# Optimization experiments

Measured on AMD Instinct MI355X. Metric: run time of the kernel, lower is better.

Reference implementation:

```python
import jax, jax.numpy as jnp
import numpy as np

D_MODEL, N_HEADS, D_K, D_V = 512, 8, 32, 32
LN_EPS = 1e-5


def setup_inputs() -> dict:
    key = jax.random.key(0)
    ks = jax.random.split(key, 12)
    B, L = 4, 2048
    inner = N_HEADS * D_K
    s_in = 1.0 / np.sqrt(D_MODEL)
    s_fc = 1.0 / np.sqrt(inner)
    return {
        "q": jax.random.normal(ks[0], (B, L, D_MODEL), jnp.float32),
        "k": jax.random.normal(ks[1], (B, L, D_MODEL), jnp.float32),
        "v": jax.random.normal(ks[2], (B, L, D_MODEL), jnp.float32),
        "Wq": jax.random.normal(ks[3], (inner, D_MODEL), jnp.float32) * s_in,
        "bq": jax.random.normal(ks[4], (inner,), jnp.float32) * 0.01,
        "Wk": jax.random.normal(ks[5], (inner, D_MODEL), jnp.float32) * s_in,
        "bk": jax.random.normal(ks[6], (inner,), jnp.float32) * 0.01,
        "Wv": jax.random.normal(ks[7], (N_HEADS * D_V, D_MODEL), jnp.float32) * s_in,
        "bv": jax.random.normal(ks[8], (N_HEADS * D_V,), jnp.float32) * 0.01,
        "Wfc": jax.random.normal(ks[9], (D_MODEL, N_HEADS * D_V), jnp.float32) * s_fc,
        "bfc": jax.random.normal(ks[10], (D_MODEL,), jnp.float32) * 0.01,
        "gamma": jnp.ones((D_MODEL,), jnp.float32),
        "beta": jnp.zeros((D_MODEL,), jnp.float32),
    }


def reference(q, k, v, Wq, bq, Wk, bk, Wv, bv, Wfc, bfc, gamma, beta):
    n, l, _ = q.shape
    # Projection output interpreted as (..., d_k, n_heads): head idx is fastest dim
    def split_heads(x, W, b, dh):
        p = x @ W.T + b                     # [n, l, dh*H]
        return p.reshape(n, x.shape[1], dh, N_HEADS).transpose(0, 3, 1, 2)  # [n,H,l,dh]

    qh = split_heads(q, Wq, bq, D_K)
    kh = split_heads(k, Wk, bk, D_K)
    vh = split_heads(v, Wv, bv, D_V)

    scale = 1.0 / jnp.sqrt(jnp.asarray(D_K, q.dtype))
    scores = jnp.einsum('nhqd,nhkd->nhqk', qh, kh) * scale  # [n,H,L,L]
    att = jax.nn.softmax(scores, axis=-1)
    out = jnp.einsum('nhqk,nhkd->nhqd', att, vh)             # [n,H,L,d_v]
    out = out.transpose(0, 2, 1, 3).reshape(n, l, N_HEADS * D_V)

    fc = out @ Wfc.T + bfc
    x = fc + q  # residual
    mean = jnp.mean(x, axis=-1, keepdims=True)
    var = jnp.mean(jnp.square(x - mean), axis=-1, keepdims=True)
    return gamma * (x - mean) / jnp.sqrt(var + LN_EPS) + beta
```

## Files before the change

kernel.cpp:

```cpp
#include <hip/hip_runtime.h>
#include <math.h>

constexpr int Bn = 4, Ln = 2048, DM = 512, NH = 8, DKv = 32, INNER = 256;
constexpr int TTOK = Bn * Ln;
constexpr size_t HEAD_ELEMS = (size_t)Bn * NH * Ln * DKv;


typedef short short8 __attribute__((ext_vector_type(8)));
typedef short short4v __attribute__((ext_vector_type(4)));
typedef float floatx4 __attribute__((ext_vector_type(4)));
typedef float floatx16 __attribute__((ext_vector_type(16)));

constexpr size_t WB_OFF  = 12536832;
constexpr size_t WFCB_OFF = WB_OFF + 3 * 131072;

constexpr float C1 = 0.25505654f;

__device__ inline short f2bf(float x) {
  unsigned u = __builtin_bit_cast(unsigned, x);
  unsigned r = (u + 0x7FFFu + ((u >> 16) & 1u)) >> 16;
  return (short)r;
}

__global__ __launch_bounds__(256) void cvtw_kernel(
    const float* __restrict__ Wq, const float* __restrict__ Wk,
    const float* __restrict__ Wv, const float* __restrict__ Wfc,
    short* __restrict__ Wb, short* __restrict__ Wfcb)
{
  const int z = blockIdx.y;
  const float* src = z == 0 ? Wq : (z == 1 ? Wk : (z == 2 ? Wv : Wfc));
  short* dst = z < 3 ? Wb + (size_t)z * 131072 : Wfcb;
  const int idx = (blockIdx.x * 256 + threadIdx.x) * 4;
  float4 x = *(const float4*)&src[idx];
  *(short4v*)&dst[idx] = (short4v){f2bf(x.x), f2bf(x.y), f2bf(x.z), f2bf(x.w)};
}

__global__ __launch_bounds__(256) void proj_kernel(
    const float* __restrict__ q, const float* __restrict__ k, const float* __restrict__ v,
    const short* __restrict__ Wb,
    const float* __restrict__ bq, const float* __restrict__ bk,
    const float* __restrict__ bv,
    short* __restrict__ ws)
{
  const int mat = blockIdx.y;
  const float* X    = mat == 0 ? q  : (mat == 1 ? k  : v);
  const short* W    = Wb + (size_t)mat * 131072;
  const float* bias = mat == 0 ? bq : (mat == 1 ? bk : bv);
  short* outp = ws + (size_t)mat * HEAD_ELEMS;

  const int t0 = blockIdx.x * 64;
  const int tid = threadIdx.x;
  const int col = tid & 15;
  const int quad = (tid & 63) >> 4;
  const int w = tid >> 6;

  __shared__ short smem[23040];
  short* Xs  = smem;
  short* Wsh = smem + 64 * 72;

  floatx16 accv;
  floatx4 acc[16];
#pragma unroll
  for (int nj = 0; nj < 16; ++nj) acc[nj] = (floatx4){0.f, 0.f, 0.f, 0.f};
  (void)accv;

  float4 xr[4];
  short8 wr[8];
  auto loadX = [&](int k0) {
#pragma unroll
    for (int j = 0; j < 4; ++j) {
      const int i = tid + j * 256, row = i >> 4, c4 = i & 15;
      xr[j] = *(const float4*)&X[(size_t)(t0 + row) * DM + k0 + c4 * 4];
    }
  };
  auto loadW = [&](int k0) {
#pragma unroll
    for (int j = 0; j < 8; ++j) {
      const int s = tid + j * 256, jrow = s >> 3, c8 = s & 7;
      const int wrow = ((jrow & 31) << 3) + (jrow >> 5);
      wr[j] = *(const short8*)&W[(size_t)wrow * DM + k0 + c8 * 8];
    }
  };

  loadX(0);
  loadW(0);

  for (int kc = 0; kc < 8; ++kc) {
#pragma unroll
    for (int j = 0; j < 4; ++j) {
      const int i = tid + j * 256, row = i >> 4, c4 = i & 15;
      *(short4v*)&Xs[row * 72 + c4 * 4] =
          (short4v){f2bf(xr[j].x), f2bf(xr[j].y), f2bf(xr[j].z), f2bf(xr[j].w)};
    }
#pragma unroll
    for (int j = 0; j < 8; ++j) {
      const int s = tid + j * 256, jrow = s >> 3, c8 = s & 7;
      *(short8*)&Wsh[jrow * 72 + c8 * 8] = wr[j];
    }
    __syncthreads();
    if (kc < 7) {
      loadX((kc + 1) * 64);
      loadW((kc + 1) * 64);
    }
#pragma unroll
    for (int ks = 0; ks < 2; ++ks) {
      short8 a = *(const short8*)&Xs[(w * 16 + col) * 72 + ks * 32 + quad * 8];
#pragma unroll
      for (int nj = 0; nj < 16; ++nj) {
        short8 b = *(const short8*)&Wsh[(nj * 16 + col) * 72 + ks * 32 + quad * 8];
        acc[nj] = __builtin_amdgcn_mfma_f32_16x16x32_bf16(a, b, acc[nj], 0, 0, 0);
      }
    }
    __syncthreads();
  }

  short* Ct = smem;
  const int n = t0 >> 11, llb = t0 & (Ln - 1);

  if (mat < 2) {
#pragma unroll
    for (int nj = 0; nj < 16; ++nj) {
      const int j = nj * 16 + col;
      const int c = ((j & 31) << 3) + (j >> 5);
      const float bi = bias[c];
#pragma unroll
      for (int r = 0; r < 4; ++r) {
        float pv = acc[nj][r] + bi;
        if (mat == 0) pv *= C1;
        Ct[(w * 16 + quad * 4 + r) * 268 + j] = f2bf(pv);
      }
    }
    __syncthreads();
#pragma unroll
    for (int it = 0; it < 8; ++it) {
      const int cid = tid + it * 256;
      const int h = cid >> 8, tok = (cid >> 2) & 63, o = cid & 3;
      short8 val = *(const short8*)&Ct[tok * 268 + h * 32 + o * 8];
      *(short8*)&outp[((size_t)(n * NH + h) * Ln + llb + tok) * DKv + o * 8] = val;
    }
  } else {
#pragma unroll
    for (int nj = 0; nj < 16; ++nj) {
      const int j = nj * 16 + col;
      const int c = ((j & 31) << 3) + (j >> 5);
      const float bi = bias[c];
      short4v pk = (short4v){f2bf(acc[nj][0] + bi), f2bf(acc[nj][1] + bi),
                             f2bf(acc[nj][2] + bi), f2bf(acc[nj][3] + bi)};
      *(short4v*)&Ct[j * 72 + w * 16 + quad * 4] = pk;
    }
    __syncthreads();
#pragma unroll
    for (int it = 0; it < 8; ++it) {
      const int cid = tid + it * 256;
      const int j = cid >> 3, to = cid & 7;
      const int h = j >> 5, d = j & 31;
      short8 val = *(const short8*)&Ct[j * 72 + to * 8];
      *(short8*)&outp[((size_t)(n * NH + h) * DKv + d) * Ln + llb + to * 8] = val;
    }
  }
}

__global__ __launch_bounds__(256) void attn_kernel(const short* __restrict__ ws,
                                                   short* __restrict__ O2b)
{
  const int vid = blockIdx.x + 16 * blockIdx.y;
  const int xcd = vid & 7, jj = vid >> 3;
  const int bh = xcd * 4 + (jj >> 4);
  const int qblk = jj & 15;

  const int n = bh >> 3, h = bh & 7;
  const int tid = threadIdx.x;
  const int lane = tid & 63;
  const int col = lane & 31;
  const int hf = lane >> 5;
  const int w = tid >> 6;
  const int qi = qblk * 128 + w * 32 + col;

  const short* Qh = ws;
  const short* Kg = ws + HEAD_ELEMS + (size_t)bh * Ln * DKv;
  const short* Vg = ws + 2 * HEAD_ELEMS + (size_t)bh * DKv * Ln;

  __shared__ short Ks[2][128 * 40];
  __shared__ short Vs[2][32 * 136];

  short8 aq[2];
#pragma unroll
  for (int c = 0; c < 2; ++c)
    aq[c] = *(const short8*)&Qh[(size_t)bh * Ln * DKv + (size_t)qi * DKv + c * 16 + hf * 8];

  short8 ones;
#pragma unroll
  for (int j = 0; j < 8; ++j) ones[j] = (short)0x3F80;

  floatx16 o, ol;
#pragma unroll
  for (int i = 0; i < 16; ++i) { o[i] = 0.f; ol[i] = 0.f; }

  const int kg = tid >> 1, khalf = tid & 1;
  const int krow = (kg & ~12) | ((kg & 4) << 1) | ((kg & 8) >> 1);
  const int kst = krow * 40 + khalf * 16;
  const int vd = tid >> 3, vkb = tid & 7;
  const int vst = vd * 136 + vkb * 16;

  short8 kr0 = *(const short8*)(Kg + kg * 32 + khalf * 16);
  short8 kr1 = *(const short8*)(Kg + kg * 32 + khalf * 16 + 8);
  short8 vr0 = *(const short8*)(Vg + (size_t)vd * Ln + vkb * 16);
  short8 vr1 = *(const short8*)(Vg + (size_t)vd * Ln + vkb * 16 + 8);

  for (int kt = 0; kt < 16; ++kt) {
    short* ksb = Ks[kt & 1];
    short* vsb = Vs[kt & 1];
    *(short8*)&ksb[kst] = kr0;
    *(short8*)&ksb[kst + 8] = kr1;
    *(short8*)&vsb[vst] = vr0;
    *(short8*)&vsb[vst + 8] = vr1;
    __syncthreads();
    if (kt < 15) {
      kr0 = *(const short8*)(Kg + (size_t)(kt + 1) * 4096 + kg * 32 + khalf * 16);
      kr1 = *(const short8*)(Kg + (size_t)(kt + 1) * 4096 + kg * 32 + khalf * 16 + 8);
      vr0 = *(const short8*)(Vg + (size_t)vd * Ln + (kt + 1) * 128 + vkb * 16);
      vr1 = *(const short8*)(Vg + (size_t)vd * Ln + (kt + 1) * 128 + vkb * 16 + 8);
    }

#pragma unroll
    for (int cc = 0; cc < 4; ++cc) {
      floatx16 st;
#pragma unroll
      for (int i = 0; i < 16; ++i) st[i] = 0.f;
      short8 kf0 = *(const short8*)&ksb[(cc * 32 + col) * 40 + hf * 8];
      short8 kf1 = *(const short8*)&ksb[(cc * 32 + col) * 40 + 16 + hf * 8];
      st = __builtin_amdgcn_mfma_f32_32x32x16_bf16(kf0, aq[0], st, 0, 0, 0);
      st = __builtin_amdgcn_mfma_f32_32x32x16_bf16(kf1, aq[1], st, 0, 0, 0);

      float p[16];
#pragma unroll
      for (int i = 0; i < 16; ++i) p[i] = __builtin_amdgcn_exp2f(st[i]);
      short8 pf[2];
#pragma unroll
      for (int half = 0; half < 2; ++half) {
        unsigned u[4];
#pragma unroll
        for (int j = 0; j < 4; ++j)
          u[j] = __builtin_amdgcn_perm(
              __builtin_bit_cast(unsigned, p[half * 8 + 2 * j + 1]),
              __builtin_bit_cast(unsigned, p[half * 8 + 2 * j]), 0x07060302u);
        uint4 uu = make_uint4(u[0], u[1], u[2], u[3]);
        pf[half] = __builtin_bit_cast(short8, uu);
      }

      ol = __builtin_amdgcn_mfma_f32_32x32x16_bf16(ones, pf[0], ol, 0, 0, 0);
      ol = __builtin_amdgcn_mfma_f32_32x32x16_bf16(ones, pf[1], ol, 0, 0, 0);

      short8 va0 = *(const short8*)&vsb[col * 136 + cc * 32 + hf * 8];
      short8 va1 = *(const short8*)&vsb[col * 136 + cc * 32 + 16 + hf * 8];
      o = __builtin_amdgcn_mfma_f32_32x32x16_bf16(va0, pf[0], o, 0, 0, 0);
      o = __builtin_amdgcn_mfma_f32_32x32x16_bf16(va1, pf[1], o, 0, 0, 0);
    }
  }

  const float inv = 1.f / ol[0];
  short* dst = &O2b[((size_t)n * Ln + qi) * INNER + h * DKv];
#pragma unroll
  for (int g4 = 0; g4 < 4; ++g4) {
    short4v pk = (short4v){f2bf(o[g4 * 4 + 0] * inv), f2bf(o[g4 * 4 + 1] * inv),
                           f2bf(o[g4 * 4 + 2] * inv), f2bf(o[g4 * 4 + 3] * inv)};
    *(short4v*)&dst[8 * g4 + 4 * hf] = pk;
  }
}

__global__ __launch_bounds__(256) void fcln_kernel(
    const short* __restrict__ O2b, const short* __restrict__ Wfcb,
    const float* __restrict__ bfc, const float* __restrict__ qin,
    const float* __restrict__ gamma, const float* __restrict__ beta,
    float* __restrict__ outp)
{
  const int t0 = blockIdx.x * 16;
  const int tid = threadIdx.x;
  const int col = tid & 15;
  const int quad = (tid & 63) >> 4;
  const int w = tid >> 6;

  __shared__ short As[16 * 264];
  __shared__ float sred[2][16][4];

  {
    const int row = tid >> 4, k16 = tid & 15;
    *(short8*)&As[row * 264 + k16 * 16] =
        *(const short8*)&O2b[(size_t)(t0 + row) * INNER + k16 * 16];
    *(short8*)&As[row * 264 + k16 * 16 + 8] =
        *(const short8*)&O2b[(size_t)(t0 + row) * INNER + k16 * 16 + 8];
  }
  __syncthreads();

  const short* Wp = Wfcb + (size_t)(w * 128 + col) * INNER + quad * 8;

  floatx4 acc[8];
#pragma unroll
  for (int nj = 0; nj < 8; ++nj) acc[nj] = (floatx4){0.f, 0.f, 0.f, 0.f};

#pragma unroll
  for (int ks = 0; ks < 8; ++ks) {
    short8 a = *(const short8*)&As[col * 264 + ks * 32 + quad * 8];
#pragma unroll
    for (int nj = 0; nj < 8; ++nj) {
      short8 b = *(const short8*)&Wp[(size_t)nj * 16 * INNER + ks * 32];
      acc[nj] = __builtin_amdgcn_mfma_f32_16x16x32_bf16(a, b, acc[nj], 0, 0, 0);
    }
  }

  float s1[4], s2[4];
#pragma unroll
  for (int r = 0; r < 4; ++r) { s1[r] = 0.f; s2[r] = 0.f; }

#pragma unroll
  for (int nj = 0; nj < 8; ++nj) {
    const int c = w * 128 + nj * 16 + col;
    const float bi = bfc[c];
#pragma unroll
    for (int r = 0; r < 4; ++r) {
      const int t = t0 + quad * 4 + r;
      float x = acc[nj][r] + bi + qin[(size_t)t * DM + c];
      acc[nj][r] = x;
      s1[r] += x;
      s2[r] += x * x;
    }
  }
#pragma unroll
  for (int r = 0; r < 4; ++r) {
#pragma unroll
    for (int off = 1; off <= 8; off <<= 1) {
      s1[r] += __shfl_xor(s1[r], off);
      s2[r] += __shfl_xor(s2[r], off);
    }
  }
  if (col == 0) {
#pragma unroll
    for (int r = 0; r < 4; ++r) {
      sred[0][quad * 4 + r][w] = s1[r];
      sred[1][quad * 4 + r][w] = s2[r];
    }
  }
  __syncthreads();

  float mean[4], rstd[4];
#pragma unroll
  for (int r = 0; r < 4; ++r) {
    const int tk = quad * 4 + r;
    const float S1 = sred[0][tk][0] + sred[0][tk][1] + sred[0][tk][2] + sred[0][tk][3];
    const float S2 = sred[1][tk][0] + sred[1][tk][1] + sred[1][tk][2] + sred[1][tk][3];
    mean[r] = S1 * (1.f / 512.f);
    const float var = S2 * (1.f / 512.f) - mean[r] * mean[r];
    rstd[r] = rsqrtf(var + 1e-5f);
  }

#pragma unroll
  for (int nj = 0; nj < 8; ++nj) {
    const int c = w * 128 + nj * 16 + col;
    const float g = gamma[c], bb = beta[c];
#pragma unroll
    for (int r = 0; r < 4; ++r) {
      const int t = t0 + quad * 4 + r;
      outp[(size_t)t * DM + c] = g * (acc[nj][r] - mean[r]) * rstd[r] + bb;
    }
  }
}

extern "C" void kernel_launch(void* const* d_in, const int* in_sizes, int n_in,
                              void* d_out, int out_size, void* d_ws, size_t ws_size,
                              hipStream_t stream) {
  const float* q     = (const float*)d_in[0];
  const float* k     = (const float*)d_in[1];
  const float* v     = (const float*)d_in[2];
  const float* Wq    = (const float*)d_in[3];
  const float* bq    = (const float*)d_in[4];
  const float* Wk    = (const float*)d_in[5];
  const float* bk    = (const float*)d_in[6];
  const float* Wv    = (const float*)d_in[7];
  const float* bv    = (const float*)d_in[8];
  const float* Wfc   = (const float*)d_in[9];
  const float* bfc   = (const float*)d_in[10];
  const float* gamma = (const float*)d_in[11];
  const float* beta  = (const float*)d_in[12];

  short* wsS  = (short*)d_ws;
  short* O2b  = wsS + 3 * HEAD_ELEMS;
  short* Wb   = wsS + WB_OFF;
  short* Wfcb = wsS + WFCB_OFF;

  cvtw_kernel<<<dim3(128, 4), 256, 0, stream>>>(Wq, Wk, Wv, Wfc, Wb, Wfcb);

  dim3 gp(TTOK / 64, 3);
  proj_kernel<<<gp, 256, 0, stream>>>(q, k, v, Wb, bq, bk, bv, wsS);

  dim3 gatt(Ln / 128, Bn * NH);
  attn_kernel<<<gatt, 256, 0, stream>>>(wsS, O2b);

  fcln_kernel<<<dim3(TTOK / 16), 256, 0, stream>>>(O2b, Wfcb, bfc, q, gamma, beta,
                                                   (float*)d_out);
}
```

Baseline: 174.5 us.

## Fuse four kernels into one cooperative persistent kernel with grid syncs

Replaces the weight-convert, projection, attention and FC+LayerNorm launches with a single cooperative kernel of 512 blocks that runs the four stages in sequence, separated by grid-wide barriers. Block indices are remapped per stage, and the attention stage spreads heads across XCDs. The aim is to remove launch gaps and tail effects between kernels. In exchange, every stage is limited to 512 blocks, and the grid syncs add barrier cost. If the cooperative launch fails, the code falls back to the old four-kernel path.

```diff
diff --git a/kernel.cpp b/kernel.cpp
--- a/kernel.cpp
+++ b/kernel.cpp
@@ -1,5 +1,8 @@
 #include <hip/hip_runtime.h>
+#include <hip/hip_cooperative_groups.h>
 #include <math.h>
+
+namespace cg = cooperative_groups;
 
 constexpr int Bn = 4, Ln = 2048, DM = 512, NH = 8, DKv = 32, INNER = 256;
 constexpr int TTOK = Bn * Ln;
@@ -20,6 +23,354 @@
   unsigned u = __builtin_bit_cast(unsigned, x);
   unsigned r = (u + 0x7FFFu + ((u >> 16) & 1u)) >> 16;
   return (short)r;
+}
+
+__global__ __launch_bounds__(256, 2) void mega_kernel(
+    const float* __restrict__ q, const float* __restrict__ kin,
+    const float* __restrict__ vin,
+    const float* __restrict__ Wq, const float* __restrict__ Wk,
+    const float* __restrict__ Wv, const float* __restrict__ Wfc,
+    const float* __restrict__ bq, const float* __restrict__ bk,
+    const float* __restrict__ bv, const float* __restrict__ bfc,
+    const float* __restrict__ gamma, const float* __restrict__ beta,
+    short* __restrict__ wsS, float* __restrict__ outp)
+{
+  cg::grid_group grid = cg::this_grid();
+  const int u = blockIdx.x;
+  const int tid = threadIdx.x;
+
+  short* Wb   = wsS + WB_OFF;
+  short* Wfcb = wsS + WFCB_OFF;
+  short* O2b  = wsS + 3 * HEAD_ELEMS;
+
+  __shared__ __align__(16) short smem[23040];
+
+  {
+    const int z = u >> 7, xb = u & 127;
+    const float* src = z == 0 ? Wq : (z == 1 ? Wk : (z == 2 ? Wv : Wfc));
+    short* dst = z < 3 ? Wb + (size_t)z * 131072 : Wfcb;
+    const int idx = (xb * 256 + tid) * 4;
+    float4 x = *(const float4*)&src[idx];
+    *(short4v*)&dst[idx] = (short4v){f2bf(x.x), f2bf(x.y), f2bf(x.z), f2bf(x.w)};
+  }
+  grid.sync();
+
+  if (u < 384) {
+    const int mat = u >> 7;
+    const int t0 = (u & 127) * 64;
+    const float* X    = mat == 0 ? q  : (mat == 1 ? kin : vin);
+    const short* W    = Wb + (size_t)mat * 131072;
+    const float* bias = mat == 0 ? bq : (mat == 1 ? bk : bv);
+    short* outph = wsS + (size_t)mat * HEAD_ELEMS;
+
+    const int col = tid & 15;
+    const int quad = (tid & 63) >> 4;
+    const int w = tid >> 6;
+
+    short* Xs  = smem;
+    short* Wsh = smem + 64 * 72;
+
+    floatx4 acc[16];
+#pragma unroll
+    for (int nj = 0; nj < 16; ++nj) acc[nj] = (floatx4){0.f, 0.f, 0.f, 0.f};
+
+    float4 xr[4];
+    short8 wr[8];
+    auto loadX = [&](int k0) {
+#pragma unroll
+      for (int j = 0; j < 4; ++j) {
+        const int i = tid + j * 256, row = i >> 4, c4 = i & 15;
+        xr[j] = *(const float4*)&X[(size_t)(t0 + row) * DM + k0 + c4 * 4];
+      }
+    };
+    auto loadW = [&](int k0) {
+#pragma unroll
+      for (int j = 0; j < 8; ++j) {
+        const int s = tid + j * 256, jrow = s >> 3, c8 = s & 7;
+        const int wrow = ((jrow & 31) << 3) + (jrow >> 5);
+        wr[j] = *(const short8*)&W[(size_t)wrow * DM + k0 + c8 * 8];
+      }
+    };
+
+    loadX(0);
+    loadW(0);
+
+    for (int kc = 0; kc < 8; ++kc) {
+#pragma unroll
+      for (int j = 0; j < 4; ++j) {
+        const int i = tid + j * 256, row = i >> 4, c4 = i & 15;
+        *(short4v*)&Xs[row * 72 + c4 * 4] =
+            (short4v){f2bf(xr[j].x), f2bf(xr[j].y), f2bf(xr[j].z), f2bf(xr[j].w)};
+      }
+#pragma unroll
+      for (int j = 0; j < 8; ++j) {
+        const int s = tid + j * 256, jrow = s >> 3, c8 = s & 7;
+        *(short8*)&Wsh[jrow * 72 + c8 * 8] = wr[j];
+      }
+      __syncthreads();
+      if (kc < 7) {
+        loadX((kc + 1) * 64);
+        loadW((kc + 1) * 64);
+      }
+#pragma unroll
+      for (int ks = 0; ks < 2; ++ks) {
+        short8 a = *(const short8*)&Xs[(w * 16 + col) * 72 + ks * 32 + quad * 8];
+#pragma unroll
+        for (int nj = 0; nj < 16; ++nj) {
+          short8 b = *(const short8*)&Wsh[(nj * 16 + col) * 72 + ks * 32 + quad * 8];
+          acc[nj] = __builtin_amdgcn_mfma_f32_16x16x32_bf16(a, b, acc[nj], 0, 0, 0);
+        }
+      }
+      __syncthreads();
+    }
+
+    short* Ct = smem;
+    const int n = t0 >> 11, llb = t0 & (Ln - 1);
+
+    if (mat < 2) {
+#pragma unroll
+      for (int nj = 0; nj < 16; ++nj) {
+        const int j = nj * 16 + col;
+        const int c = ((j & 31) << 3) + (j >> 5);
+        const float bi = bias[c];
+#pragma unroll
+        for (int r = 0; r < 4; ++r) {
+          float pv = acc[nj][r] + bi;
+          if (mat == 0) pv *= C1;
+          Ct[(w * 16 + quad * 4 + r) * 268 + j] = f2bf(pv);
+        }
+      }
+      __syncthreads();
+#pragma unroll
+      for (int it = 0; it < 8; ++it) {
+        const int cid = tid + it * 256;
+        const int h = cid >> 8, tok = (cid >> 2) & 63, o = cid & 3;
+        short8 val = *(const short8*)&Ct[tok * 268 + h * 32 + o * 8];
+        *(short8*)&outph[((size_t)(n * NH + h) * Ln + llb + tok) * DKv + o * 8] = val;
+      }
+    } else {
+#pragma unroll
+      for (int nj = 0; nj < 16; ++nj) {
+        const int j = nj * 16 + col;
+        const int c = ((j & 31) << 3) + (j >> 5);
+        const float bi = bias[c];
+        short4v pk = (short4v){f2bf(acc[nj][0] + bi), f2bf(acc[nj][1] + bi),
+                               f2bf(acc[nj][2] + bi), f2bf(acc[nj][3] + bi)};
+        *(short4v*)&Ct[j * 72 + w * 16 + quad * 4] = pk;
+      }
+      __syncthreads();
+#pragma unroll
+      for (int it = 0; it < 8; ++it) {
+        const int cid = tid + it * 256;
+        const int j = cid >> 3, to = cid & 7;
+        const int h = j >> 5, d = j & 31;
+        short8 val = *(const short8*)&Ct[j * 72 + to * 8];
+        *(short8*)&outph[((size_t)(n * NH + h) * DKv + d) * Ln + llb + to * 8] = val;
+      }
+    }
+  }
+  grid.sync();
+
+  {
+    const int vid = u;
+    const int xcd = vid & 7, jj = vid >> 3;
+    const int bh = xcd * 4 + (jj >> 4);
+    const int qblk = jj & 15;
+
+    const int n = bh >> 3, h = bh & 7;
+    const int lane = tid & 63;
+    const int col = lane & 31;
+    const int hf = lane >> 5;
+    const int w = tid >> 6;
+    const int qi = qblk * 128 + w * 32 + col;
+
+    const short* Qh = wsS;
+    const short* Kg = wsS + HEAD_ELEMS + (size_t)bh * Ln * DKv;
+    const short* Vg = wsS + 2 * HEAD_ELEMS + (size_t)bh * DKv * Ln;
+
+    short8 aq[2];
+#pragma unroll
+    for (int c = 0; c < 2; ++c)
+      aq[c] = *(const short8*)&Qh[(size_t)bh * Ln * DKv + (size_t)qi * DKv + c * 16 + hf * 8];
+
+    short8 ones;
+#pragma unroll
+    for (int j = 0; j < 8; ++j) ones[j] = (short)0x3F80;
+
+    floatx16 o, ol;
+#pragma unroll
+    for (int i = 0; i < 16; ++i) { o[i] = 0.f; ol[i] = 0.f; }
+
+    const int kg = tid >> 1, khalf = tid & 1;
+    const int krow = (kg & ~12) | ((kg & 4) << 1) | ((kg & 8) >> 1);
+    const int kst = krow * 40 + khalf * 16;
+    const int vd = tid >> 3, vkb = tid & 7;
+    const int vst = vd * 136 + vkb * 16;
+
+    short8 kr0 = *(const short8*)(Kg + kg * 32 + khalf * 16);
+    short8 kr1 = *(const short8*)(Kg + kg * 32 + khalf * 16 + 8);
+    short8 vr0 = *(const short8*)(Vg + (size_t)vd * Ln + vkb * 16);
+    short8 vr1 = *(const short8*)(Vg + (size_t)vd * Ln + vkb * 16 + 8);
+
+    for (int kt = 0; kt < 16; ++kt) {
+      short* ksb = smem + (kt & 1) * 5120;
+      short* vsb = smem + 10240 + (kt & 1) * 4352;
+      *(short8*)&ksb[kst] = kr0;
+      *(short8*)&ksb[kst + 8] = kr1;
+      *(short8*)&vsb[vst] = vr0;
+      *(short8*)&vsb[vst + 8] = vr1;
+      __syncthreads();
+      if (kt < 15) {
+        kr0 = *(const short8*)(Kg + (size_t)(kt + 1) * 4096 + kg * 32 + khalf * 16);
+        kr1 = *(const short8*)(Kg + (size_t)(kt + 1) * 4096 + kg * 32 + khalf * 16 + 8);
+        vr0 = *(const short8*)(Vg + (size_t)vd * Ln + (kt + 1) * 128 + vkb * 16);
+        vr1 = *(const short8*)(Vg + (size_t)vd * Ln + (kt + 1) * 128 + vkb * 16 + 8);
+      }
+
+#pragma unroll
+      for (int cc = 0; cc < 4; ++cc) {
+        floatx16 st;
+#pragma unroll
+        for (int i = 0; i < 16; ++i) st[i] = 0.f;
+        short8 kf0 = *(const short8*)&ksb[(cc * 32 + col) * 40 + hf * 8];
+        short8 kf1 = *(const short8*)&ksb[(cc * 32 + col) * 40 + 16 + hf * 8];
+        st = __builtin_amdgcn_mfma_f32_32x32x16_bf16(kf0, aq[0], st, 0, 0, 0);
+        st = __builtin_amdgcn_mfma_f32_32x32x16_bf16(kf1, aq[1], st, 0, 0, 0);
+
+        float p[16];
+#pragma unroll
+        for (int i = 0; i < 16; ++i) p[i] = __builtin_amdgcn_exp2f(st[i]);
+        short8 pf[2];
+#pragma unroll
+        for (int half = 0; half < 2; ++half) {
+          unsigned uu0 = __builtin_amdgcn_perm(
+              __builtin_bit_cast(unsigned, p[half * 8 + 1]),
+              __builtin_bit_cast(unsigned, p[half * 8 + 0]), 0x07060302u);
+          unsigned uu1 = __builtin_amdgcn_perm(
+              __builtin_bit_cast(unsigned, p[half * 8 + 3]),
+              __builtin_bit_cast(unsigned, p[half * 8 + 2]), 0x07060302u);
+          unsigned uu2 = __builtin_amdgcn_perm(
+              __builtin_bit_cast(unsigned, p[half * 8 + 5]),
+              __builtin_bit_cast(unsigned, p[half * 8 + 4]), 0x07060302u);
+          unsigned uu3 = __builtin_amdgcn_perm(
+              __builtin_bit_cast(unsigned, p[half * 8 + 7]),
+              __builtin_bit_cast(unsigned, p[half * 8 + 6]), 0x07060302u);
+          uint4 uu = make_uint4(uu0, uu1, uu2, uu3);
+          pf[half] = __builtin_bit_cast(short8, uu);
+        }
+
+        ol = __builtin_amdgcn_mfma_f32_32x32x16_bf16(ones, pf[0], ol, 0, 0, 0);
+        ol = __builtin_amdgcn_mfma_f32_32x32x16_bf16(ones, pf[1], ol, 0, 0, 0);
+
+        short8 va0 = *(const short8*)&vsb[col * 136 + cc * 32 + hf * 8];
+        short8 va1 = *(const short8*)&vsb[col * 136 + cc * 32 + 16 + hf * 8];
+        o = __builtin_amdgcn_mfma_f32_32x32x16_bf16(va0, pf[0], o, 0, 0, 0);
+        o = __builtin_amdgcn_mfma_f32_32x32x16_bf16(va1, pf[1], o, 0, 0, 0);
+      }
+    }
+
+    const float inv = 1.f / ol[0];
+    short* dst = &O2b[((size_t)n * Ln + qi) * INNER + h * DKv];
+#pragma unroll
+    for (int g4 = 0; g4 < 4; ++g4) {
+      short4v pk = (short4v){f2bf(o[g4 * 4 + 0] * inv), f2bf(o[g4 * 4 + 1] * inv),
+                             f2bf(o[g4 * 4 + 2] * inv), f2bf(o[g4 * 4 + 3] * inv)};
+      *(short4v*)&dst[8 * g4 + 4 * hf] = pk;
+    }
+  }
+  grid.sync();
+
+  {
+    const int t0 = u * 16;
+    const int col = tid & 15;
+    const int quad = (tid & 63) >> 4;
+    const int w = tid >> 6;
+
+    short* As = smem;
+    float* sred = (float*)(smem + 4224);
+
+    {
+      const int row = tid >> 4, k16 = tid & 15;
+      *(short8*)&As[row * 264 + k16 * 16] =
+          *(const short8*)&O2b[(size_t)(t0 + row) * INNER + k16 * 16];
+      *(short8*)&As[row * 264 + k16 * 16 + 8] =
+          *(const short8*)&O2b[(size_t)(t0 + row) * INNER + k16 * 16 + 8];
+    }
+    __syncthreads();
+
+    const short* Wp = Wfcb + (size_t)(w * 128 + col) * INNER + quad * 8;
+
+    floatx4 acc[8];
+#pragma unroll
+    for (int nj = 0; nj < 8; ++nj) acc[nj] = (floatx4){0.f, 0.f, 0.f, 0.f};
+
+#pragma unroll
+    for (int ks = 0; ks < 8; ++ks) {
+      short8 a = *(const short8*)&As[col * 264 + ks * 32 + quad * 8];
+#pragma unroll
+      for (int nj = 0; nj < 8; ++nj) {
+        short8 b = *(const short8*)&Wp[(size_t)nj * 16 * INNER + ks * 32];
+        acc[nj] = __builtin_amdgcn_mfma_f32_16x16x32_bf16(a, b, acc[nj], 0, 0, 0);
+      }
+    }
+
+    float s1[4], s2[4];
+#pragma unroll
+    for (int r = 0; r < 4; ++r) { s1[r] = 0.f; s2[r] = 0.f; }
+
+#pragma unroll
+    for (int nj = 0; nj < 8; ++nj) {
+      const int c = w * 128 + nj * 16 + col;
+      const float bi = bfc[c];
+#pragma unroll
+      for (int r = 0; r < 4; ++r) {
+        const int t = t0 + quad * 4 + r;
+        float x = acc[nj][r] + bi + q[(size_t)t * DM + c];
+        acc[nj][r] = x;
+        s1[r] += x;
+        s2[r] += x * x;
+      }
+    }
+#pragma unroll
+    for (int r = 0; r < 4; ++r) {
+#pragma unroll
+      for (int off = 1; off <= 8; off <<= 1) {
+        s1[r] += __shfl_xor(s1[r], off);
+        s2[r] += __shfl_xor(s2[r], off);
+      }
+    }
+    if (col == 0) {
+#pragma unroll
+      for (int r = 0; r < 4; ++r) {
+        sred[(0 * 16 + quad * 4 + r) * 4 + w] = s1[r];
+        sred[(1 * 16 + quad * 4 + r) * 4 + w] = s2[r];
+      }
+    }
+    __syncthreads();
+
+    float mean[4], rstd[4];
+#pragma unroll
+    for (int r = 0; r < 4; ++r) {
+      const int tk = quad * 4 + r;
+      const float S1 = sred[tk * 4 + 0] + sred[tk * 4 + 1] + sred[tk * 4 + 2] + sred[tk * 4 + 3];
+      const float S2 = sred[(16 + tk) * 4 + 0] + sred[(16 + tk) * 4 + 1] +
+                       sred[(16 + tk) * 4 + 2] + sred[(16 + tk) * 4 + 3];
+      mean[r] = S1 * (1.f / 512.f);
+      const float var = S2 * (1.f / 512.f) - mean[r] * mean[r];
+      rstd[r] = rsqrtf(var + 1e-5f);
+    }
+
+#pragma unroll
+    for (int nj = 0; nj < 8; ++nj) {
+      const int c = w * 128 + nj * 16 + col;
+      const float g = gamma[c], bb = beta[c];
+#pragma unroll
+      for (int r = 0; r < 4; ++r) {
+        const int t = t0 + quad * 4 + r;
+        outp[(size_t)t * DM + c] = g * (acc[nj][r] - mean[r]) * rstd[r] + bb;
+      }
+    }
+  }
 }
 
 __global__ __launch_bounds__(256) void cvtw_kernel(
@@ -58,11 +409,9 @@
   short* Xs  = smem;
   short* Wsh = smem + 64 * 72;
 
-  floatx16 accv;
   floatx4 acc[16];
 #pragma unroll
   for (int nj = 0; nj < 16; ++nj) acc[nj] = (floatx4){0.f, 0.f, 0.f, 0.f};
-  (void)accv;
 
   float4 xr[4];
   short8 wr[8];
@@ -238,13 +587,13 @@
       short8 pf[2];
 #pragma unroll
       for (int half = 0; half < 2; ++half) {
-        unsigned u[4];
+        unsigned uarr[4];
 #pragma unroll
         for (int j = 0; j < 4; ++j)
-          u[j] = __builtin_amdgcn_perm(
+          uarr[j] = __builtin_amdgcn_perm(
               __builtin_bit_cast(unsigned, p[half * 8 + 2 * j + 1]),
               __builtin_bit_cast(unsigned, p[half * 8 + 2 * j]), 0x07060302u);
-        uint4 uu = make_uint4(u[0], u[1], u[2], u[3]);
+        uint4 uu = make_uint4(uarr[0], uarr[1], uarr[2], uarr[3]);
         pf[half] = __builtin_bit_cast(short8, uu);
       }
 
@@ -386,15 +735,24 @@
   short* O2b  = wsS + 3 * HEAD_ELEMS;
   short* Wb   = wsS + WB_OFF;
   short* Wfcb = wsS + WFCB_OFF;
-
-  cvtw_kernel<<<dim3(128, 4), 256, 0, stream>>>(Wq, Wk, Wv, Wfc, Wb, Wfcb);
-
-  dim3 gp(TTOK / 64, 3);
-  proj_kernel<<<gp, 256, 0, stream>>>(q, k, v, Wb, bq, bk, bv, wsS);
-
-  dim3 gatt(Ln / 128, Bn * NH);
-  attn_kernel<<<gatt, 256, 0, stream>>>(wsS, O2b);
-
-  fcln_kernel<<<dim3(TTOK / 16), 256, 0, stream>>>(O2b, Wfcb, bfc, q, gamma, beta,
-                                                   (float*)d_out);
+  float* outP = (float*)d_out;
+
+  void* kargs[] = {(void*)&q,  (void*)&k,  (void*)&v,
+                   (void*)&Wq, (void*)&Wk, (void*)&Wv, (void*)&Wfc,
+                   (void*)&bq, (void*)&bk, (void*)&bv, (void*)&bfc,
+                   (void*)&gamma, (void*)&beta,
+                   (void*)&wsS, (void*)&outP};
+  hipError_t err = hipLaunchCooperativeKernel(
+      reinterpret_cast<void*>(mega_kernel), dim3(512), dim3(256), kargs, 0, stream);
+
+  if (err != hipSuccess) {
+    (void)hipGetLastError();
+    cvtw_kernel<<<dim3(128, 4), 256, 0, stream>>>(Wq, Wk, Wv, Wfc, Wb, Wfcb);
+    dim3 gp(TTOK / 64, 3);
+    proj_kernel<<<gp, 256, 0, stream>>>(q, k, v, Wb, bq, bk, bv, wsS);
+    dim3 gatt(Ln / 128, Bn * NH);
+    attn_kernel<<<gatt, 256, 0, stream>>>(wsS, O2b);
+    fcln_kernel<<<dim3(TTOK / 16), 256, 0, stream>>>(O2b, Wfcb, bfc, q, gamma, beta,
+                                                     outP);
+  }
 }
```

Measured after the change: 372.6 us. +113.4%, slower.

## Split projection kernel output columns across 4 blocks per token tile

Applied to the files above, without the earlier changes.

The QKV projection kernel now launches a 3D grid where each block computes only 64 of the 256 output columns (two heads) for its 64-token tile, instead of all 256. This cuts per-block accumulators, shared memory and register use, giving 4x more blocks and higher occupancy. The cost is that each X tile (fp32 load plus bf16 conversion) is now read and converted four times. The attention kernel's perm loop is also unrolled by hand, which is cosmetic.

```diff
diff --git a/kernel.cpp b/kernel.cpp
--- a/kernel.cpp
+++ b/kernel.cpp
@@ -42,7 +42,8 @@
     const float* __restrict__ bv,
     short* __restrict__ ws)
 {
-  const int mat = blockIdx.y;
+  const int mat = blockIdx.z;
+  const int cp  = blockIdx.y;
   const float* X    = mat == 0 ? q  : (mat == 1 ? k  : v);
   const short* W    = Wb + (size_t)mat * 131072;
   const float* bias = mat == 0 ? bq : (mat == 1 ? bk : bv);
@@ -54,18 +55,16 @@
   const int quad = (tid & 63) >> 4;
   const int w = tid >> 6;
 
-  __shared__ short smem[23040];
+  __shared__ short smem[9216];
   short* Xs  = smem;
   short* Wsh = smem + 64 * 72;
 
-  floatx16 accv;
-  floatx4 acc[16];
-#pragma unroll
-  for (int nj = 0; nj < 16; ++nj) acc[nj] = (floatx4){0.f, 0.f, 0.f, 0.f};
-  (void)accv;
+  floatx4 acc[4];
+#pragma unroll
+  for (int nj = 0; nj < 4; ++nj) acc[nj] = (floatx4){0.f, 0.f, 0.f, 0.f};
 
   float4 xr[4];
-  short8 wr[8];
+  short8 wr[2];
   auto loadX = [&](int k0) {
 #pragma unroll
     for (int j = 0; j < 4; ++j) {
@@ -75,9 +74,9 @@
   };
   auto loadW = [&](int k0) {
 #pragma unroll
-    for (int j = 0; j < 8; ++j) {
+    for (int j = 0; j < 2; ++j) {
       const int s = tid + j * 256, jrow = s >> 3, c8 = s & 7;
-      const int wrow = ((jrow & 31) << 3) + (jrow >> 5);
+      const int wrow = ((jrow & 31) << 3) + 2 * cp + (jrow >> 5);
       wr[j] = *(const short8*)&W[(size_t)wrow * DM + k0 + c8 * 8];
     }
   };
@@ -93,7 +92,7 @@
           (short4v){f2bf(xr[j].x), f2bf(xr[j].y), f2bf(xr[j].z), f2bf(xr[j].w)};
     }
 #pragma unroll
-    for (int j = 0; j < 8; ++j) {
+    for (int j = 0; j < 2; ++j) {
       const int s = tid + j * 256, jrow = s >> 3, c8 = s & 7;
       *(short8*)&Wsh[jrow * 72 + c8 * 8] = wr[j];
     }
@@ -106,7 +105,7 @@
     for (int ks = 0; ks < 2; ++ks) {
       short8 a = *(const short8*)&Xs[(w * 16 + col) * 72 + ks * 32 + quad * 8];
 #pragma unroll
-      for (int nj = 0; nj < 16; ++nj) {
+      for (int nj = 0; nj < 4; ++nj) {
         short8 b = *(const short8*)&Wsh[(nj * 16 + col) * 72 + ks * 32 + quad * 8];
         acc[nj] = __builtin_amdgcn_mfma_f32_16x16x32_bf16(a, b, acc[nj], 0, 0, 0);
       }
@@ -119,30 +118,31 @@
 
   if (mat < 2) {
 #pragma unroll
-    for (int nj = 0; nj < 16; ++nj) {
+    for (int nj = 0; nj < 4; ++nj) {
       const int j = nj * 16 + col;
-      const int c = ((j & 31) << 3) + (j >> 5);
+      const int c = ((j & 31) << 3) + 2 * cp + (j >> 5);
       const float bi = bias[c];
 #pragma unroll
       for (int r = 0; r < 4; ++r) {
         float pv = acc[nj][r] + bi;
         if (mat == 0) pv *= C1;
-        Ct[(w * 16 + quad * 4 + r) * 268 + j] = f2bf(pv);
+        Ct[(w * 16 + quad * 4 + r) * 72 + j] = f2bf(pv);
       }
     }
     __syncthreads();
 #pragma unroll
-    for (int it = 0; it < 8; ++it) {
+    for (int it = 0; it < 2; ++it) {
       const int cid = tid + it * 256;
-      const int h = cid >> 8, tok = (cid >> 2) & 63, o = cid & 3;
-      short8 val = *(const short8*)&Ct[tok * 268 + h * 32 + o * 8];
+      const int h_loc = cid >> 8, tok = (cid >> 2) & 63, o = cid & 3;
+      short8 val = *(const short8*)&Ct[tok * 72 + h_loc * 32 + o * 8];
+      const int h = 2 * cp + h_loc;
       *(short8*)&outp[((size_t)(n * NH + h) * Ln + llb + tok) * DKv + o * 8] = val;
     }
   } else {
 #pragma unroll
-    for (int nj = 0; nj < 16; ++nj) {
+    for (int nj = 0; nj < 4; ++nj) {
       const int j = nj * 16 + col;
-      const int c = ((j & 31) << 3) + (j >> 5);
+      const int c = ((j & 31) << 3) + 2 * cp + (j >> 5);
       const float bi = bias[c];
       short4v pk = (short4v){f2bf(acc[nj][0] + bi), f2bf(acc[nj][1] + bi),
                              f2bf(acc[nj][2] + bi), f2bf(acc[nj][3] + bi)};
@@ -150,10 +150,10 @@
     }
     __syncthreads();
 #pragma unroll
-    for (int it = 0; it < 8; ++it) {
+    for (int it = 0; it < 2; ++it) {
       const int cid = tid + it * 256;
       const int j = cid >> 3, to = cid & 7;
-      const int h = j >> 5, d = j & 31;
+      const int h = 2 * cp + (j >> 5), d = j & 31;
       short8 val = *(const short8*)&Ct[j * 72 + to * 8];
       *(short8*)&outp[((size_t)(n * NH + h) * DKv + d) * Ln + llb + to * 8] = val;
     }
@@ -238,13 +238,19 @@
       short8 pf[2];
 #pragma unroll
       for (int half = 0; half < 2; ++half) {
-        unsigned u[4];
-#pragma unroll
-        for (int j = 0; j < 4; ++j)
-          u[j] = __builtin_amdgcn_perm(
-              __builtin_bit_cast(unsigned, p[half * 8 + 2 * j + 1]),
-              __builtin_bit_cast(unsigned, p[half * 8 + 2 * j]), 0x07060302u);
-        uint4 uu = make_uint4(u[0], u[1], u[2], u[3]);
+        unsigned u0 = __builtin_amdgcn_perm(
+            __builtin_bit_cast(unsigned, p[half * 8 + 1]),
+            __builtin_bit_cast(unsigned, p[half * 8 + 0]), 0x07060302u);
+        unsigned u1 = __builtin_amdgcn_perm(
+            __builtin_bit_cast(unsigned, p[half * 8 + 3]),
+            __builtin_bit_cast(unsigned, p[half * 8 + 2]), 0x07060302u);
+        unsigned u2 = __builtin_amdgcn_perm(
+            __builtin_bit_cast(unsigned, p[half * 8 + 5]),
+            __builtin_bit_cast(unsigned, p[half * 8 + 4]), 0x07060302u);
+        unsigned u3 = __builtin_amdgcn_perm(
+            __builtin_bit_cast(unsigned, p[half * 8 + 7]),
+            __builtin_bit_cast(unsigned, p[half * 8 + 6]), 0x07060302u);
+        uint4 uu = make_uint4(u0, u1, u2, u3);
         pf[half] = __builtin_bit_cast(short8, uu);
       }
 
@@ -389,7 +395,7 @@
 
   cvtw_kernel<<<dim3(128, 4), 256, 0, stream>>>(Wq, Wk, Wv, Wfc, Wb, Wfcb);
 
-  dim3 gp(TTOK / 64, 3);
+  dim3 gp(TTOK / 64, 4, 3);
   proj_kernel<<<gp, 256, 0, stream>>>(q, k, v, Wb, bq, bk, bv, wsS);
 
   dim3 gatt(Ln / 128, Bn * NH);
```

Result: slower. 181.9 us (+4.2%).
